# Performance work log

Hardware: AMD Instinct MI355X
Metric: run time of the kernel (lower is better)

Reference implementation:

```python
import jax, jax.numpy as jnp
import numpy as np

N = 4
TMAX = 20
EPS = 1e-06
POST_MULT = 2.0


def setup_inputs() -> dict:
    key = jax.random.key(0)
    ks = jax.random.split(key, 8)
    T, C = 8192, 1024
    return {
        "x": jax.random.normal(ks[0], (T, N, C), dtype=jnp.float32),
        "f_out": jax.random.normal(ks[1], (T, C), dtype=jnp.float32),
        "mix": jax.random.normal(ks[2], (T, 2 * N + N * N), dtype=jnp.float32),
        "invr": jax.random.uniform(ks[3], (T,), dtype=jnp.float32),
        "alpha_pre": jax.random.uniform(ks[4], (1,), dtype=jnp.float32),
        "alpha_post": jax.random.uniform(ks[5], (1,), dtype=jnp.float32),
        "alpha_res": jax.random.uniform(ks[6], (1,), dtype=jnp.float32),
        "bias": jax.random.normal(ks[7], (2 * N + N * N,), dtype=jnp.float32),
    }


def _sinkhorn(r):
    # r: (T, N, N) logits. Row-softmax exp, then TMAX row/col normalizations.
    r = jnp.exp(r - jnp.max(r, axis=-1, keepdims=True))
    def body(_, r):
        r = r / (jnp.sum(r, axis=-1, keepdims=True) + EPS)  # row normalize
        r = r / (jnp.sum(r, axis=-2, keepdims=True) + EPS)  # col normalize
        return r
    return jax.lax.fori_loop(0, TMAX, body, r)


def reference(x, f_out, mix, invr, alpha_pre, alpha_post, alpha_res, bias):
    T = mix.shape[0]
    s = mix * invr[:, None]  # (T, 24)
    h_pre = jax.nn.sigmoid(s[:, :N] * alpha_pre + bias[:N])                      # (T, N)
    h_post = jax.nn.sigmoid(s[:, N:2 * N] * alpha_post + bias[N:2 * N]) * POST_MULT  # (T, N)
    r = (s[:, 2 * N:] * alpha_res + bias[2 * N:]).reshape(T, N, N)
    h_res = _sinkhorn(r)  # (T, N, N), doubly-normalized mixing matrix
    # pre-aggregate the N residual streams into one (input to the wrapped sublayer)
    y_pre = jnp.einsum("tn,tnc->tc", h_pre, x)
    # residual remix + gated sublayer output broadcast back to N streams
    out = jnp.einsum("tji,tic->tjc", h_res, x) + h_post[:, :, None] * f_out[:, None, :]
    return y_pre, out
```

## Files before the change

### kernel.cpp

```cpp
#include <hip/hip_runtime.h>
#include <math.h>

#define NN 4
#define TMAX 20
#define EPS 1e-6f
#define POST_MULT 2.0f

typedef float vfloat4 __attribute__((ext_vector_type(4)));

__global__ __launch_bounds__(256) void coeff_kernel(
    const float* __restrict__ mix,
    const float* __restrict__ invr,
    const float* __restrict__ alpha_pre,
    const float* __restrict__ alpha_post,
    const float* __restrict__ alpha_res,
    const float* __restrict__ bias,
    float* __restrict__ coeffs,
    int T)
{
    const int gtid = blockIdx.x * blockDim.x + threadIdx.x;
    const int t    = gtid >> 4;
    const int lane = gtid & 15;
    if (t >= T) return;

    const float ir = invr[t];

    float r = mix[t * 24 + 8 + lane] * ir * alpha_res[0] + bias[8 + lane];
    float m = r;
    m = fmaxf(m, __shfl_xor(m, 1));
    m = fmaxf(m, __shfl_xor(m, 2));
    r = __expf(r - m);
    #pragma unroll
    for (int it = 0; it < TMAX; ++it) {
        float rs = r;
        rs += __shfl_xor(rs, 1);
        rs += __shfl_xor(rs, 2);
        r = r / (rs + EPS);
        float cs = r;
        cs += __shfl_xor(cs, 4);
        cs += __shfl_xor(cs, 8);
        r = r / (cs + EPS);
    }
    coeffs[t * 24 + 8 + lane] = r;

    if (lane < 8) {
        const float a = (lane < NN) ? alpha_pre[0] : alpha_post[0];
        const float z = mix[t * 24 + lane] * ir * a + bias[lane];
        float sg = 1.0f / (1.0f + __expf(-z));
        if (lane >= NN) sg *= POST_MULT;
        coeffs[t * 24 + lane] = sg;
    }
}

__global__ __launch_bounds__(256) void stream_kernel(
    const float* __restrict__ x,
    const float* __restrict__ f_out,
    const float* __restrict__ coeffs,
    float* __restrict__ y_pre,
    float* __restrict__ out,
    int C)
{
    const int t   = blockIdx.x;
    const int tid = threadIdx.x;

    const float* cf = coeffs + (size_t)t * 24;
    const float hp0 = cf[0], hp1 = cf[1], hp2 = cf[2], hp3 = cf[3];
    const float hq0 = cf[4], hq1 = cf[5], hq2 = cf[6], hq3 = cf[7];
    float hr[NN][NN];
    #pragma unroll
    for (int j = 0; j < NN; ++j)
        #pragma unroll
        for (int i = 0; i < NN; ++i)
            hr[j][i] = cf[8 + j * 4 + i];

    const int NV = C >> 2;
    const vfloat4* xv4 = (const vfloat4*)(x + (size_t)t * NN * C);
    const vfloat4* fv4 = (const vfloat4*)(f_out + (size_t)t * C);
    vfloat4* yp4 = (vfloat4*)(y_pre + (size_t)t * C);
    vfloat4* o4  = (vfloat4*)(out + (size_t)t * NN * C);

    for (int v = tid; v < NV; v += blockDim.x) {
        vfloat4 xv[NN];
        #pragma unroll
        for (int n = 0; n < NN; ++n) xv[n] = xv4[n * NV + v];
        const vfloat4 fv = fv4[v];

        vfloat4 yv = hp0 * xv[0] + hp1 * xv[1] + hp2 * xv[2] + hp3 * xv[3];
        __builtin_nontemporal_store(yv, &yp4[v]);

        const float hq[NN] = {hq0, hq1, hq2, hq3};
        #pragma unroll
        for (int j = 0; j < NN; ++j) {
            vfloat4 ov = hq[j] * fv;
            #pragma unroll
            for (int i = 0; i < NN; ++i) ov += hr[j][i] * xv[i];
            __builtin_nontemporal_store(ov, &o4[j * NV + v]);
        }
    }
}

extern "C" void kernel_launch(void* const* d_in, const int* in_sizes, int n_in,
                              void* d_out, int out_size, void* d_ws, size_t ws_size,
                              hipStream_t stream) {
    const float* x          = (const float*)d_in[0];
    const float* f_out      = (const float*)d_in[1];
    const float* mix        = (const float*)d_in[2];
    const float* invr       = (const float*)d_in[3];
    const float* alpha_pre  = (const float*)d_in[4];
    const float* alpha_post = (const float*)d_in[5];
    const float* alpha_res  = (const float*)d_in[6];
    const float* bias       = (const float*)d_in[7];

    const int T = in_sizes[3];
    const int C = in_sizes[1] / T;

    float* y_pre = (float*)d_out;
    float* out   = (float*)d_out + (size_t)T * C;
    float* coeffs = (float*)d_ws;

    const int grid1 = (T * 16 + 255) / 256;
    coeff_kernel<<<grid1, 256, 0, stream>>>(mix, invr, alpha_pre, alpha_post,
                                            alpha_res, bias, coeffs, T);
    stream_kernel<<<T, 256, 0, stream>>>(x, f_out, coeffs, y_pre, out, C);
}
```

Measured before the change: 303.8 us.

## Use grid-stride persistent stream kernel processing two far-apart items per iteration

Replaces the one-block-per-token stream kernel with a fixed 2048-block grid-stride kernel over flattened (token, vector) items. Each thread handles two items half the problem apart per iteration, so more loads are in flight, and the coefficient loads use a wave-uniform token index via readfirstlane. The aim is to cut block launch overhead and raise memory-level parallelism on this bandwidth-bound kernel. A fallback path keeps the old kernel for non-power-of-two C or odd T.

```diff
diff --git a/kernel.cpp b/kernel.cpp
--- a/kernel.cpp
+++ b/kernel.cpp
@@ -52,26 +52,71 @@
     }
 }
 
+__device__ __forceinline__ void process_item(
+    long i, int sh, int NV,
+    const float* __restrict__ x, const float* __restrict__ f_out,
+    const float* __restrict__ coeffs,
+    float* __restrict__ y_pre, float* __restrict__ out)
+{
+    const int t = (int)(i >> sh);
+    const int v = (int)(i & (NV - 1));
+
+    const int ts = __builtin_amdgcn_readfirstlane(t);
+    const float* cf = coeffs + (size_t)ts * 24;
+
+    const vfloat4* xv4 = (const vfloat4*)x + (size_t)t * NN * NV;
+    const vfloat4* fv4 = (const vfloat4*)f_out + (size_t)t * NV;
+    vfloat4* yp4 = (vfloat4*)y_pre + (size_t)t * NV;
+    vfloat4* o4  = (vfloat4*)out + (size_t)t * NN * NV;
+
+    vfloat4 xv[NN];
+    #pragma unroll
+    for (int n = 0; n < NN; ++n) xv[n] = xv4[n * NV + v];
+    const vfloat4 fv = fv4[v];
+
+    vfloat4 yv = cf[0] * xv[0] + cf[1] * xv[1] + cf[2] * xv[2] + cf[3] * xv[3];
+    __builtin_nontemporal_store(yv, &yp4[v]);
+
+    #pragma unroll
+    for (int j = 0; j < NN; ++j) {
+        vfloat4 ov = cf[4 + j] * fv;
+        #pragma unroll
+        for (int ii = 0; ii < NN; ++ii) ov += cf[8 + j * 4 + ii] * xv[ii];
+        __builtin_nontemporal_store(ov, &o4[j * NV + v]);
+    }
+}
+
 __global__ __launch_bounds__(256) void stream_kernel(
     const float* __restrict__ x,
     const float* __restrict__ f_out,
     const float* __restrict__ coeffs,
     float* __restrict__ y_pre,
     float* __restrict__ out,
-    int C)
+    int C, int T)
+{
+    const int NV = C >> 2;
+    const int sh = 31 - __clz(NV);
+    const long M = (long)T << sh;
+    const long half = M >> 1;
+    const long stride = (long)gridDim.x * blockDim.x;
+    const long gid = (long)blockIdx.x * blockDim.x + threadIdx.x;
+
+    for (long i = gid; i < half; i += stride) {
+        process_item(i,        sh, NV, x, f_out, coeffs, y_pre, out);
+        process_item(i + half, sh, NV, x, f_out, coeffs, y_pre, out);
+    }
+    for (long i = (half << 1) + gid; i < M; i += stride)
+        process_item(i, sh, NV, x, f_out, coeffs, y_pre, out);
+}
+
+__global__ __launch_bounds__(256) void stream_fallback(
+    const float* __restrict__ x, const float* __restrict__ f_out,
+    const float* __restrict__ coeffs,
+    float* __restrict__ y_pre, float* __restrict__ out, int C)
 {
     const int t   = blockIdx.x;
     const int tid = threadIdx.x;
-
     const float* cf = coeffs + (size_t)t * 24;
-    const float hp0 = cf[0], hp1 = cf[1], hp2 = cf[2], hp3 = cf[3];
-    const float hq0 = cf[4], hq1 = cf[5], hq2 = cf[6], hq3 = cf[7];
-    float hr[NN][NN];
-    #pragma unroll
-    for (int j = 0; j < NN; ++j)
-        #pragma unroll
-        for (int i = 0; i < NN; ++i)
-            hr[j][i] = cf[8 + j * 4 + i];
 
     const int NV = C >> 2;
     const vfloat4* xv4 = (const vfloat4*)(x + (size_t)t * NN * C);
@@ -85,15 +130,14 @@
         for (int n = 0; n < NN; ++n) xv[n] = xv4[n * NV + v];
         const vfloat4 fv = fv4[v];
 
-        vfloat4 yv = hp0 * xv[0] + hp1 * xv[1] + hp2 * xv[2] + hp3 * xv[3];
+        vfloat4 yv = cf[0] * xv[0] + cf[1] * xv[1] + cf[2] * xv[2] + cf[3] * xv[3];
         __builtin_nontemporal_store(yv, &yp4[v]);
 
-        const float hq[NN] = {hq0, hq1, hq2, hq3};
         #pragma unroll
         for (int j = 0; j < NN; ++j) {
-            vfloat4 ov = hq[j] * fv;
+            vfloat4 ov = cf[4 + j] * fv;
             #pragma unroll
-            for (int i = 0; i < NN; ++i) ov += hr[j][i] * xv[i];
+            for (int i = 0; i < NN; ++i) ov += cf[8 + j * 4 + i] * xv[i];
             __builtin_nontemporal_store(ov, &o4[j * NV + v]);
         }
     }
@@ -121,5 +165,14 @@
     const int grid1 = (T * 16 + 255) / 256;
     coeff_kernel<<<grid1, 256, 0, stream>>>(mix, invr, alpha_pre, alpha_post,
                                             alpha_res, bias, coeffs, T);
-    stream_kernel<<<T, 256, 0, stream>>>(x, f_out, coeffs, y_pre, out, C);
+
+    const int NV = C >> 2;
+    const bool fast = NV > 0 && (NV & (NV - 1)) == 0 && (NV % 64) == 0
+                      && (T % 2) == 0;
+    if (fast) {
+        stream_kernel<<<2048, 256, 0, stream>>>(x, f_out, coeffs, y_pre, out,
+                                                C, T);
+    } else {
+        stream_fallback<<<T, 256, 0, stream>>>(x, f_out, coeffs, y_pre, out, C);
+    }
 }
```

Measured after the change: 302.6 us. No clear change (-0.4%).
